# Optimization experiments

Measured on AMD Instinct MI355X. Metric: run time of the kernel, lower is better.

## Reference

```python
import jax, jax.numpy as jnp
import numpy as np

N_NODES = 100000
N_EDGES = 3200000
DIMS = [64, 64, 32, 16]  # [embedding_size] + conv_dim_list
LN_EPS = 1e-5


def _xavier(key, shape):
    fan_in, fan_out = shape[0], shape[1]
    s = np.sqrt(6.0 / (fan_in + fan_out)).astype(np.float32)
    return jax.random.uniform(key, shape, jnp.float32, -s, s)


def _layer_norm(x, g, b):
    m = jnp.mean(x, axis=-1, keepdims=True)
    v = jnp.mean((x - m) ** 2, axis=-1, keepdims=True)
    return (x - m) * jax.lax.rsqrt(v + LN_EPS) * g + b


def _bi_interaction(ego, rows, cols, vals, w1, b1, w2, b2, g1, be1, g2, be2):
    # sparse SpMM: side = A_in @ ego, A_in[rows, cols] = vals
    msg = vals[:, None] * ego[cols]                              # (E, d_in)
    side = jax.ops.segment_sum(msg, rows, num_segments=ego.shape[0])
    s = _layer_norm(jax.nn.leaky_relu((ego + side) @ w1 + b1), g1, be1)
    bi = _layer_norm(jax.nn.leaky_relu((ego * side) @ w2 + b2), g2, be2)
    return s + bi


def _l2_normalize(x):
    n = jnp.sqrt(jnp.sum(x * x, axis=1, keepdims=True))
    return x / jnp.maximum(n, 1e-12)


def setup_inputs() -> dict:
    key = jax.random.key(0)
    ks = jax.random.split(key, 32)
    inp = {
        "emb": jax.random.normal(ks[0], (N_NODES, DIMS[0]), jnp.float32) * 0.1,
        "rows": jax.random.randint(ks[1], (N_EDGES,), 0, N_NODES, jnp.int32),
        "cols": jax.random.randint(ks[2], (N_EDGES,), 0, N_NODES, jnp.int32),
        "vals": jax.random.uniform(ks[3], (N_EDGES,), jnp.float32),
    }
    i = 4
    for k in range(3):
        din, dout = DIMS[k], DIMS[k + 1]
        inp[f"w1_{k}"] = _xavier(ks[i], (din, dout)); i += 1
        inp[f"b1_{k}"] = jnp.zeros((dout,), jnp.float32)
        inp[f"w2_{k}"] = _xavier(ks[i], (din, dout)); i += 1
        inp[f"b2_{k}"] = jnp.zeros((dout,), jnp.float32)
        inp[f"g1_{k}"] = jnp.ones((dout,), jnp.float32)
        inp[f"be1_{k}"] = jnp.zeros((dout,), jnp.float32)
        inp[f"g2_{k}"] = jnp.ones((dout,), jnp.float32)
        inp[f"be2_{k}"] = jnp.zeros((dout,), jnp.float32)
    return inp


def reference(emb, rows, cols, vals,
              w1_0, b1_0, w2_0, b2_0, g1_0, be1_0, g2_0, be2_0,
              w1_1, b1_1, w2_1, b2_1, g1_1, be1_1, g2_1, be2_1,
              w1_2, b1_2, w2_2, b2_2, g1_2, be1_2, g2_2, be2_2):
    layers = [
        (w1_0, b1_0, w2_0, b2_0, g1_0, be1_0, g2_0, be2_0),
        (w1_1, b1_1, w2_1, b2_1, g1_1, be1_1, g2_1, be2_1),
        (w1_2, b1_2, w2_2, b2_2, g1_2, be1_2, g2_2, be2_2),
    ]
    ego = emb
    all_embed = [ego]
    for p in layers:
        ego = _bi_interaction(ego, rows, cols, vals, *p)
        all_embed.append(_l2_normalize(ego))
    return jnp.concatenate(all_embed, axis=1)  # (N, 64+64+32+16)
```

## Files before the change

kernel.cpp:

```cpp
#include <hip/hip_runtime.h>
#include <hip/hip_fp16.h>

#define N_NODES 100000
#define N_EDGES 3200000
#define OUT_DIM 176
#define LN_EPS 1e-5f

typedef _Float16 h2 __attribute__((ext_vector_type(2)));

#define NBUCK 196
#define PC_BLOCKS 512
#define PC_CHUNK (N_EDGES / PC_BLOCKS)
#define BP_CHUNK 4096
#define BP_BLOCKS ((N_EDGES + BP_CHUNK - 1) / BP_CHUNK)

__global__ __launch_bounds__(256) void convert_emb_kernel(
    const float* __restrict__ emb, float* __restrict__ out,
    __half* __restrict__ emb_h) {
  int t = blockIdx.x * blockDim.x + threadIdx.x;
  if (t < N_NODES * 16) {
    int n = t >> 4, q = t & 15;
    float4 v = ((const float4*)emb)[t];
    ((float4*)out)[n * 44 + q] = v;
    __half2 a = __floats2half2_rn(v.x, v.y);
    __half2 b = __floats2half2_rn(v.z, v.w);
    uint2 u;
    u.x = *(unsigned int*)&a;
    u.y = *(unsigned int*)&b;
    ((uint2*)emb_h)[t] = u;
  }
}

__global__ __launch_bounds__(256) void wprep_all_kernel(
    const float* __restrict__ w1_0, const float* __restrict__ w2_0,
    const float* __restrict__ w1_1, const float* __restrict__ w2_1,
    const float* __restrict__ w1_2, const float* __restrict__ w2_2,
    __half* __restrict__ wt1_0, __half* __restrict__ wt2_0,
    __half* __restrict__ wt1_1, __half* __restrict__ wt2_1,
    __half* __restrict__ wt1_2, __half* __restrict__ wt2_2) {
  int idx = blockIdx.x * 256 + threadIdx.x;
  const float* w1;
  const float* w2;
  __half* t1;
  __half* t2;
  int din, dout;
  if (idx < 4096) {
    w1 = w1_0; w2 = w2_0; t1 = wt1_0; t2 = wt2_0; din = 64; dout = 64;
  } else if (idx < 4096 + 2048) {
    idx -= 4096;
    w1 = w1_1; w2 = w2_1; t1 = wt1_1; t2 = wt2_1; din = 64; dout = 32;
  } else if (idx < 4096 + 2048 + 512) {
    idx -= 4096 + 2048;
    w1 = w1_2; w2 = w2_2; t1 = wt1_2; t2 = wt2_2; din = 32; dout = 16;
  } else {
    return;
  }
  int i = idx / dout, j = idx % dout;
  t1[j * din + i] = __float2half(w1[idx]);
  t2[j * din + i] = __float2half(w2[idx]);
}

__global__ __launch_bounds__(256) void precount_kernel(
    const int* __restrict__ rows, int* __restrict__ gcount) {
  __shared__ int hist[NBUCK];
  for (int i = threadIdx.x; i < NBUCK; i += 256) hist[i] = 0;
  __syncthreads();
  const int e0 = blockIdx.x * PC_CHUNK;
  for (int e = e0 + threadIdx.x; e < e0 + PC_CHUNK; e += 256) {
    const int r = __builtin_nontemporal_load(rows + e);
    atomicAdd(&hist[r >> 9], 1);
  }
  __syncthreads();
  for (int i = threadIdx.x; i < NBUCK; i += 256)
    if (hist[i]) atomicAdd(&gcount[i], hist[i]);
}

__global__ __launch_bounds__(256) void bucket_scan_kernel(
    const int* __restrict__ gcount, int* __restrict__ bucket_base,
    int* __restrict__ bucket_cursor) {
  __shared__ int sA[256], sB[256];
  const int t = threadIdx.x;
  int v = (t < NBUCK) ? gcount[t] : 0;
  sA[t] = v;
  __syncthreads();
  int* src = sA;
  int* dst = sB;
  for (int off = 1; off < 256; off <<= 1) {
    dst[t] = src[t] + ((t >= off) ? src[t - off] : 0);
    __syncthreads();
    int* tmp = src; src = dst; dst = tmp;
  }
  if (t < NBUCK) {
    const int excl = src[t] - v;
    bucket_base[t] = excl;
    bucket_cursor[t] = excl;
  }
  if (t == 0) bucket_base[NBUCK] = N_EDGES;
}

__global__ __launch_bounds__(256) void bucket_pass_kernel(
    const int* __restrict__ rows, const int* __restrict__ cols,
    const float* __restrict__ vals, int* __restrict__ bucket_cursor,
    int2* __restrict__ bucketed) {
  __shared__ int cnt[NBUCK], cur[NBUCK], gbase[NBUCK];
  for (int i = threadIdx.x; i < NBUCK; i += 256) {
    cnt[i] = 0;
    cur[i] = 0;
  }
  __syncthreads();

  const int e0 = blockIdx.x * BP_CHUNK;
  int r_[16], c_[16];
  float v_[16];
#pragma unroll
  for (int k = 0; k < 16; ++k) {
    const int e = e0 + threadIdx.x + k * 256;
    if (e < N_EDGES) {
      r_[k] = rows[e];
      c_[k] = cols[e];
      v_[k] = vals[e];
      atomicAdd(&cnt[r_[k] >> 9], 1);
    } else {
      r_[k] = -1;
    }
  }
  __syncthreads();

  for (int i = threadIdx.x; i < NBUCK; i += 256)
    gbase[i] = cnt[i] ? atomicAdd(&bucket_cursor[i], cnt[i]) : 0;
  __syncthreads();

#pragma unroll
  for (int k = 0; k < 16; ++k) {
    if (r_[k] >= 0) {
      const int b = r_[k] >> 9;
      const int lp = atomicAdd(&cur[b], 1);
      const int meta = c_[k] | ((r_[k] & 511) << 17);
      bucketed[gbase[b] + lp] = make_int2(meta, __float_as_int(v_[k]));
    }
  }
}

__global__ __launch_bounds__(512) void csr_build_kernel(
    const int2* __restrict__ bucketed, const int* __restrict__ bucket_base,
    int* __restrict__ row_ptr, int2* __restrict__ packed) {
  __shared__ int hist[512], cur[512], sA[512], sB[512];
  const int t = threadIdx.x;
  const int blk = blockIdx.x;
  const int base = bucket_base[blk];
  const int n = bucket_base[blk + 1] - base;

  hist[t] = 0;
  __syncthreads();
  for (int i = t; i < n; i += 512) {
    const int rlow = bucketed[base + i].x >> 17;
    atomicAdd(&hist[rlow], 1);
  }
  __syncthreads();

  sA[t] = hist[t];
  __syncthreads();
  int* src = sA;
  int* dst = sB;
  for (int off = 1; off < 512; off <<= 1) {
    dst[t] = src[t] + ((t >= off) ? src[t - off] : 0);
    __syncthreads();
    int* tmp = src; src = dst; dst = tmp;
  }
  const int excl = src[t] - hist[t];

  const int row0 = blk << 9;
  if (row0 + t < N_NODES) row_ptr[row0 + t] = base + excl;
  if (blk == NBUCK - 1 && t == 0) row_ptr[N_NODES] = N_EDGES;
  cur[t] = excl;
  __syncthreads();

  for (int i = t; i < n; i += 512) {
    const int2 m = bucketed[base + i];
    const int rlow = m.x >> 17;
    const int col = m.x & 0x1FFFF;
    const int p = atomicAdd(&cur[rlow], 1);
    packed[base + p] = make_int2(col, m.y);
  }
}

template <int DIN>
__global__ __launch_bounds__(512) void spmm_kernel(
    const __half* __restrict__ ego_h, const int* __restrict__ row_ptr,
    const long long* __restrict__ packed, __half* __restrict__ side_out_h) {
  constexpr int LPH = DIN / 8;
  constexpr int NGRP = 64 / LPH;

  const int lane = threadIdx.x & 63;
  const int li = lane % LPH;
  const int grp = lane / LPH;
  const int node = (blockIdx.x * blockDim.x + threadIdx.x) >> 6;
  if (node >= N_NODES) return;

  const uint4* __restrict__ ego8 = (const uint4*)ego_h;
  const int start = row_ptr[node];
  const int end = row_ptr[node + 1];

  float s[8] = {0.f, 0.f, 0.f, 0.f, 0.f, 0.f, 0.f, 0.f};

  for (int base = start; base < end; base += 64) {
    const int idx = base + lane;
    long long m = 0;
    if (idx < end) m = __builtin_nontemporal_load(packed + idx);
    int mc = (int)m;
    int mv = (int)(m >> 32);
    const int cnt = min(end - base, 64);
    const int kmax = (cnt + NGRP - 1) / NGRP;
    for (int k = 0; k < kmax; ++k) {
      const int src = k * NGRP + grp;
      const int c = __shfl(mc, src, 64);
      const float v = __int_as_float(__shfl(mv, src, 64));
      uint4 raw = ego8[(long)c * LPH + li];
      const __half2* hp = (const __half2*)&raw;
      const float2 f0 = __half22float2(hp[0]);
      const float2 f1 = __half22float2(hp[1]);
      const float2 f2 = __half22float2(hp[2]);
      const float2 f3 = __half22float2(hp[3]);
      s[0] += v * f0.x; s[1] += v * f0.y;
      s[2] += v * f1.x; s[3] += v * f1.y;
      s[4] += v * f2.x; s[5] += v * f2.y;
      s[6] += v * f3.x; s[7] += v * f3.y;
    }
  }

#pragma unroll
  for (int mask = LPH; mask < 64; mask <<= 1) {
#pragma unroll
    for (int r = 0; r < 8; ++r) s[r] += __shfl_xor(s[r], mask, 64);
  }

  if (grp == 0) {
    __half2 p0 = __floats2half2_rn(s[0], s[1]);
    __half2 p1 = __floats2half2_rn(s[2], s[3]);
    __half2 p2 = __floats2half2_rn(s[4], s[5]);
    __half2 p3 = __floats2half2_rn(s[6], s[7]);
    uint4 u;
    u.x = *(unsigned int*)&p0;
    u.y = *(unsigned int*)&p1;
    u.z = *(unsigned int*)&p2;
    u.w = *(unsigned int*)&p3;
    ((uint4*)side_out_h)[(long)node * LPH + li] = u;
  }
}

template <int DIN, int DOUT, int COL_OFF>
__global__ __launch_bounds__(256, 4) void dense_kernel(
    const __half* __restrict__ ego_h, const __half* __restrict__ side_h,
    const __half* __restrict__ w1t, const float* __restrict__ b1,
    const __half* __restrict__ w2t, const float* __restrict__ b2,
    const float* __restrict__ g1, const float* __restrict__ be1,
    const float* __restrict__ g2, const float* __restrict__ be2,
    __half* __restrict__ ego_h_out, float* __restrict__ out) {
  constexpr int CH = DIN / 8;
  constexpr int G = 64 / CH;
  constexpr int NPW = 64 / DOUT;
  constexpr int PASSES = G / NPW;

  const int lane = threadIdx.x & 63;
  const int w = threadIdx.x >> 6;
  const int j = lane % DOUT;
  const int sub = lane / DOUT;
  const int sn = lane / CH;
  const int sc = lane % CH;

  __shared__ uint4 lds[4][2][64];

  const uint4* __restrict__ w1u = (const uint4*)w1t;
  const uint4* __restrict__ w2u = (const uint4*)w2t;
  uint4 wraw1[CH], wraw2[CH];
#pragma unroll
  for (int q = 0; q < CH; ++q) {
    wraw1[q] = w1u[j * CH + q];
    wraw2[q] = w2u[j * CH + q];
  }
  const float bb1 = b1[j], bb2 = b2[j];
  const float gg1 = g1[j], gg2 = g2[j];
  const float bbe1 = be1[j], bbe2 = be2[j];

  const uint4* __restrict__ ego8 = (const uint4*)ego_h;
  const uint4* __restrict__ side8 = (const uint4*)side_h;

  const int waveId = (blockIdx.x * blockDim.x + threadIdx.x) >> 6;
  const int nwaves = (gridDim.x * blockDim.x) >> 6;
  const int ngangs = N_NODES / G;

  uint4 eR, sR;
  if (waveId < ngangs) {
    const size_t b = (size_t)(waveId * G + sn) * CH + sc;
    eR = ego8[b];
    sR = side8[b];
  }

  for (int gang = waveId; gang < ngangs; gang += nwaves) {
    uint4 xsU, xpU;
    {
      const h2* e2 = (const h2*)&eR;
      const h2* s2 = (const h2*)&sR;
      h2* xs2 = (h2*)&xsU;
      h2* xp2 = (h2*)&xpU;
#pragma unroll
      for (int r = 0; r < 4; ++r) {
        xs2[r] = e2[r] + s2[r];
        xp2[r] = e2[r] * s2[r];
      }
    }
    asm volatile("s_waitcnt lgkmcnt(0)" ::: "memory");
    __builtin_amdgcn_sched_barrier(0);
    lds[w][0][lane] = xsU;
    lds[w][1][lane] = xpU;

    const int gn = gang + nwaves;
    if (gn < ngangs) {
      const size_t b = (size_t)(gn * G + sn) * CH + sc;
      eR = ego8[b];
      sR = side8[b];
    }

    asm volatile("s_waitcnt lgkmcnt(0)" ::: "memory");
    __builtin_amdgcn_sched_barrier(0);

#pragma unroll
    for (int p = 0; p < PASSES; ++p) {
      const int nin = p * NPW + sub;
      const int node = gang * G + nin;

      float a1a = bb1, a1b = 0.f, a2a = bb2, a2b = 0.f;
#pragma unroll
      for (int q = 0; q < CH; ++q) {
        uint4 xsq = lds[w][0][nin * CH + q];
        uint4 xpq = lds[w][1][nin * CH + q];
        const h2* xs2 = (const h2*)&xsq;
        const h2* xp2 = (const h2*)&xpq;
        const h2* wq1 = (const h2*)&wraw1[q];
        const h2* wq2 = (const h2*)&wraw2[q];
#pragma unroll
        for (int r = 0; r < 4; ++r) {
#if __has_builtin(__builtin_amdgcn_fdot2)
          if (q & 1) {
            a1b = __builtin_amdgcn_fdot2(xs2[r], wq1[r], a1b, false);
            a2b = __builtin_amdgcn_fdot2(xp2[r], wq2[r], a2b, false);
          } else {
            a1a = __builtin_amdgcn_fdot2(xs2[r], wq1[r], a1a, false);
            a2a = __builtin_amdgcn_fdot2(xp2[r], wq2[r], a2a, false);
          }
#else
          if (q & 1) {
            a1b += (float)xs2[r].x * (float)wq1[r].x +
                   (float)xs2[r].y * (float)wq1[r].y;
            a2b += (float)xp2[r].x * (float)wq2[r].x +
                   (float)xp2[r].y * (float)wq2[r].y;
          } else {
            a1a += (float)xs2[r].x * (float)wq1[r].x +
                   (float)xs2[r].y * (float)wq1[r].y;
            a2a += (float)xp2[r].x * (float)wq2[r].x +
                   (float)xp2[r].y * (float)wq2[r].y;
          }
#endif
        }
      }

      const float acc1 = a1a + a1b;
      const float acc2 = a2a + a2b;
      const float h1 = acc1 > 0.f ? acc1 : 0.01f * acc1;
      const float h2v = acc2 > 0.f ? acc2 : 0.01f * acc2;

      float s1 = h1, q1 = h1 * h1, s2 = h2v, q2 = h2v * h2v;
#pragma unroll
      for (int mask = DOUT / 2; mask > 0; mask >>= 1) {
        s1 += __shfl_xor(s1, mask, DOUT);
        q1 += __shfl_xor(q1, mask, DOUT);
        s2 += __shfl_xor(s2, mask, DOUT);
        q2 += __shfl_xor(q2, mask, DOUT);
      }
      const float m1 = s1 * (1.0f / DOUT);
      const float m2 = s2 * (1.0f / DOUT);
      const float v1 = fmaxf(q1 * (1.0f / DOUT) - m1 * m1, 0.f);
      const float v2 = fmaxf(q2 * (1.0f / DOUT) - m2 * m2, 0.f);
      const float sv = (h1 - m1) * rsqrtf(v1 + LN_EPS) * gg1 + bbe1;
      const float bv = (h2v - m2) * rsqrtf(v2 + LN_EPS) * gg2 + bbe2;
      const float en = sv + bv;

      float ss = en * en;
#pragma unroll
      for (int mask = DOUT / 2; mask > 0; mask >>= 1) {
        ss += __shfl_xor(ss, mask, DOUT);
      }
      const float ov = en / fmaxf(sqrtf(ss), 1e-12f);

      if (ego_h_out) ego_h_out[(long)node * DOUT + j] = __float2half(en);
      out[(long)node * OUT_DIM + COL_OFF + j] = ov;
    }
  }
}

extern "C" void kernel_launch(void* const* d_in, const int* in_sizes, int n_in,
                              void* d_out, int out_size, void* d_ws,
                              size_t ws_size, hipStream_t stream) {
  const float* emb = (const float*)d_in[0];
  const int* rows = (const int*)d_in[1];
  const int* cols = (const int*)d_in[2];
  const float* vals = (const float*)d_in[3];

  const float* P[3][8];
  for (int k = 0; k < 3; ++k)
    for (int p = 0; p < 8; ++p) P[k][p] = (const float*)d_in[4 + 8 * k + p];

  float* out = (float*)d_out;

  char* ws = (char*)d_ws;
  int2* packed = (int2*)ws;
  char* sideArea = ws + (size_t)N_EDGES * 8;
  __half* side_h = (__half*)sideArea;
  int2* bucketed = (int2*)sideArea;
  __half* emb_h = (__half*)(sideArea + (size_t)N_NODES * 64 * 4);
  __half* ego1_h = emb_h + (size_t)N_NODES * 64;
  __half* ego2_h = ego1_h + (size_t)N_NODES * 64;
  __half* wt1_0 = ego2_h + (size_t)N_NODES * 32;
  __half* wt2_0 = wt1_0 + 4096;
  __half* wt1_1 = wt2_0 + 4096;
  __half* wt2_1 = wt1_1 + 2048;
  __half* wt1_2 = wt2_1 + 2048;
  __half* wt2_2 = wt1_2 + 512;
  int* row_ptr = (int*)(wt2_2 + 512);
  int* gcount = row_ptr + (N_NODES + 1);
  int* bucket_base = gcount + NBUCK;
  int* bucket_cursor = bucket_base + (NBUCK + 1);

  hipMemsetAsync(gcount, 0, NBUCK * sizeof(int), stream);
  precount_kernel<<<PC_BLOCKS, 256, 0, stream>>>(rows, gcount);
  bucket_scan_kernel<<<1, 256, 0, stream>>>(gcount, bucket_base,
                                            bucket_cursor);
  bucket_pass_kernel<<<BP_BLOCKS, 256, 0, stream>>>(rows, cols, vals,
                                                    bucket_cursor, bucketed);
  csr_build_kernel<<<NBUCK, 512, 0, stream>>>(bucketed, bucket_base, row_ptr,
                                              packed);

  wprep_all_kernel<<<26, 256, 0, stream>>>(P[0][0], P[0][2], P[1][0], P[1][2],
                                           P[2][0], P[2][2], wt1_0, wt2_0,
                                           wt1_1, wt2_1, wt1_2, wt2_2);

  convert_emb_kernel<<<(N_NODES * 16 + 255) / 256, 256, 0, stream>>>(emb, out,
                                                                     emb_h);

  const int SPMM_BLOCKS = (N_NODES + 7) / 8;
  const int DENSE_BLOCKS = 2048;

  spmm_kernel<64><<<SPMM_BLOCKS, 512, 0, stream>>>(
      emb_h, row_ptr, (const long long*)packed, side_h);
  dense_kernel<64, 64, 64><<<DENSE_BLOCKS, 256, 0, stream>>>(
      emb_h, side_h, wt1_0, P[0][1], wt2_0, P[0][3], P[0][4], P[0][5],
      P[0][6], P[0][7], ego1_h, out);

  spmm_kernel<64><<<SPMM_BLOCKS, 512, 0, stream>>>(
      ego1_h, row_ptr, (const long long*)packed, side_h);
  dense_kernel<64, 32, 128><<<DENSE_BLOCKS, 256, 0, stream>>>(
      ego1_h, side_h, wt1_1, P[1][1], wt2_1, P[1][3], P[1][4], P[1][5],
      P[1][6], P[1][7], ego2_h, out);

  spmm_kernel<32><<<SPMM_BLOCKS, 512, 0, stream>>>(
      ego2_h, row_ptr, (const long long*)packed, side_h);
  dense_kernel<32, 16, 160><<<DENSE_BLOCKS, 256, 0, stream>>>(
      ego2_h, side_h, wt1_2, P[2][1], wt2_2, P[2][3], P[2][4], P[2][5],
      P[2][6], P[2][7], nullptr, out);
}
```

Baseline: 536.1 us.

## Fuse SpMM and dense bi-interaction into one per-layer kernel

Merges the sparse aggregation and the dense linear/LayerNorm/L2 step into a single persistent kernel per layer. Each wave gathers neighbours for one node, combines the result with the node's embedding in registers, stages it through LDS, and runs the matvec with the weights split across lane groups, finishing with a cross-group shuffle reduction. This removes the fp16 side buffer round trip and three kernel launches. In exchange, the dense phase now processes one node per wave, so only a fraction of lanes do useful work there, and the fixed grid sizes may limit how well latency is hidden during the gather.

```diff
diff --git a/kernel.cpp b/kernel.cpp
--- a/kernel.cpp
+++ b/kernel.cpp
@@ -184,214 +184,164 @@
   }
 }
 
-template <int DIN>
-__global__ __launch_bounds__(512) void spmm_kernel(
+template <int DIN, int DOUT, int COL_OFF>
+__global__ __launch_bounds__(256, 4) void fused_layer_kernel(
     const __half* __restrict__ ego_h, const int* __restrict__ row_ptr,
-    const long long* __restrict__ packed, __half* __restrict__ side_out_h) {
+    const long long* __restrict__ packed, const __half* __restrict__ w1t,
+    const float* __restrict__ b1, const __half* __restrict__ w2t,
+    const float* __restrict__ b2, const float* __restrict__ g1,
+    const float* __restrict__ be1, const float* __restrict__ g2,
+    const float* __restrict__ be2, __half* __restrict__ ego_h_out,
+    float* __restrict__ out) {
   constexpr int LPH = DIN / 8;
   constexpr int NGRP = 64 / LPH;
+  constexpr int CH = DIN / 8;
+  constexpr int SPL = 64 / DOUT;
+  constexpr int QPS = CH / SPL;
 
   const int lane = threadIdx.x & 63;
+  const int w = threadIdx.x >> 6;
   const int li = lane % LPH;
   const int grp = lane / LPH;
-  const int node = (blockIdx.x * blockDim.x + threadIdx.x) >> 6;
-  if (node >= N_NODES) return;
-
-  const uint4* __restrict__ ego8 = (const uint4*)ego_h;
-  const int start = row_ptr[node];
-  const int end = row_ptr[node + 1];
-
-  float s[8] = {0.f, 0.f, 0.f, 0.f, 0.f, 0.f, 0.f, 0.f};
-
-  for (int base = start; base < end; base += 64) {
-    const int idx = base + lane;
-    long long m = 0;
-    if (idx < end) m = __builtin_nontemporal_load(packed + idx);
-    int mc = (int)m;
-    int mv = (int)(m >> 32);
-    const int cnt = min(end - base, 64);
-    const int kmax = (cnt + NGRP - 1) / NGRP;
-    for (int k = 0; k < kmax; ++k) {
-      const int src = k * NGRP + grp;
-      const int c = __shfl(mc, src, 64);
-      const float v = __int_as_float(__shfl(mv, src, 64));
-      uint4 raw = ego8[(long)c * LPH + li];
-      const __half2* hp = (const __half2*)&raw;
-      const float2 f0 = __half22float2(hp[0]);
-      const float2 f1 = __half22float2(hp[1]);
-      const float2 f2 = __half22float2(hp[2]);
-      const float2 f3 = __half22float2(hp[3]);
-      s[0] += v * f0.x; s[1] += v * f0.y;
-      s[2] += v * f1.x; s[3] += v * f1.y;
-      s[4] += v * f2.x; s[5] += v * f2.y;
-      s[6] += v * f3.x; s[7] += v * f3.y;
-    }
-  }
-
-#pragma unroll
-  for (int mask = LPH; mask < 64; mask <<= 1) {
-#pragma unroll
-    for (int r = 0; r < 8; ++r) s[r] += __shfl_xor(s[r], mask, 64);
-  }
-
-  if (grp == 0) {
-    __half2 p0 = __floats2half2_rn(s[0], s[1]);
-    __half2 p1 = __floats2half2_rn(s[2], s[3]);
-    __half2 p2 = __floats2half2_rn(s[4], s[5]);
-    __half2 p3 = __floats2half2_rn(s[6], s[7]);
-    uint4 u;
-    u.x = *(unsigned int*)&p0;
-    u.y = *(unsigned int*)&p1;
-    u.z = *(unsigned int*)&p2;
-    u.w = *(unsigned int*)&p3;
-    ((uint4*)side_out_h)[(long)node * LPH + li] = u;
-  }
-}
-
-template <int DIN, int DOUT, int COL_OFF>
-__global__ __launch_bounds__(256, 4) void dense_kernel(
-    const __half* __restrict__ ego_h, const __half* __restrict__ side_h,
-    const __half* __restrict__ w1t, const float* __restrict__ b1,
-    const __half* __restrict__ w2t, const float* __restrict__ b2,
-    const float* __restrict__ g1, const float* __restrict__ be1,
-    const float* __restrict__ g2, const float* __restrict__ be2,
-    __half* __restrict__ ego_h_out, float* __restrict__ out) {
-  constexpr int CH = DIN / 8;
-  constexpr int G = 64 / CH;
-  constexpr int NPW = 64 / DOUT;
-  constexpr int PASSES = G / NPW;
-
-  const int lane = threadIdx.x & 63;
-  const int w = threadIdx.x >> 6;
   const int j = lane % DOUT;
   const int sub = lane / DOUT;
-  const int sn = lane / CH;
-  const int sc = lane % CH;
-
-  __shared__ uint4 lds[4][2][64];
+
+  __shared__ uint4 lds[4][2][CH];
 
   const uint4* __restrict__ w1u = (const uint4*)w1t;
   const uint4* __restrict__ w2u = (const uint4*)w2t;
-  uint4 wraw1[CH], wraw2[CH];
-#pragma unroll
-  for (int q = 0; q < CH; ++q) {
-    wraw1[q] = w1u[j * CH + q];
-    wraw2[q] = w2u[j * CH + q];
+  uint4 wr1[QPS], wr2[QPS];
+#pragma unroll
+  for (int q = 0; q < QPS; ++q) {
+    wr1[q] = w1u[j * CH + sub * QPS + q];
+    wr2[q] = w2u[j * CH + sub * QPS + q];
+    asm volatile("" : "+v"(wr1[q].x), "+v"(wr1[q].y), "+v"(wr1[q].z),
+                      "+v"(wr1[q].w));
+    asm volatile("" : "+v"(wr2[q].x), "+v"(wr2[q].y), "+v"(wr2[q].z),
+                      "+v"(wr2[q].w));
   }
   const float bb1 = b1[j], bb2 = b2[j];
   const float gg1 = g1[j], gg2 = g2[j];
   const float bbe1 = be1[j], bbe2 = be2[j];
 
   const uint4* __restrict__ ego8 = (const uint4*)ego_h;
-  const uint4* __restrict__ side8 = (const uint4*)side_h;
 
   const int waveId = (blockIdx.x * blockDim.x + threadIdx.x) >> 6;
   const int nwaves = (gridDim.x * blockDim.x) >> 6;
-  const int ngangs = N_NODES / G;
-
-  uint4 eR, sR;
-  if (waveId < ngangs) {
-    const size_t b = (size_t)(waveId * G + sn) * CH + sc;
-    eR = ego8[b];
-    sR = side8[b];
-  }
-
-  for (int gang = waveId; gang < ngangs; gang += nwaves) {
-    uint4 xsU, xpU;
-    {
-      const h2* e2 = (const h2*)&eR;
-      const h2* s2 = (const h2*)&sR;
-      h2* xs2 = (h2*)&xsU;
-      h2* xp2 = (h2*)&xpU;
-#pragma unroll
-      for (int r = 0; r < 4; ++r) {
-        xs2[r] = e2[r] + s2[r];
-        xp2[r] = e2[r] * s2[r];
+
+  for (int node = waveId; node < N_NODES; node += nwaves) {
+    const int start = row_ptr[node];
+    const int end = row_ptr[node + 1];
+
+    float s[8] = {0.f, 0.f, 0.f, 0.f, 0.f, 0.f, 0.f, 0.f};
+    for (int base = start; base < end; base += 64) {
+      const int idx = base + lane;
+      long long m = 0;
+      if (idx < end) m = __builtin_nontemporal_load(packed + idx);
+      const int mc = (int)m;
+      const int mv = (int)(m >> 32);
+      const int cnt = min(end - base, 64);
+      const int kmax = (cnt + NGRP - 1) / NGRP;
+      for (int k = 0; k < kmax; ++k) {
+        const int src = k * NGRP + grp;
+        const int c = __shfl(mc, src, 64);
+        const float v = __int_as_float(__shfl(mv, src, 64));
+        uint4 raw = ego8[(long)c * LPH + li];
+        const __half2* hp = (const __half2*)&raw;
+        const float2 f0 = __half22float2(hp[0]);
+        const float2 f1 = __half22float2(hp[1]);
+        const float2 f2 = __half22float2(hp[2]);
+        const float2 f3 = __half22float2(hp[3]);
+        s[0] += v * f0.x; s[1] += v * f0.y;
+        s[2] += v * f1.x; s[3] += v * f1.y;
+        s[4] += v * f2.x; s[5] += v * f2.y;
+        s[6] += v * f3.x; s[7] += v * f3.y;
       }
     }
+
+    uint4 eg = make_uint4(0, 0, 0, 0);
+    if (grp == 0) eg = ego8[(long)node * CH + li];
+
+#pragma unroll
+    for (int mask = LPH; mask < 64; mask <<= 1)
+#pragma unroll
+      for (int r = 0; r < 8; ++r) s[r] += __shfl_xor(s[r], mask, 64);
+
     asm volatile("s_waitcnt lgkmcnt(0)" ::: "memory");
     __builtin_amdgcn_sched_barrier(0);
-    lds[w][0][lane] = xsU;
-    lds[w][1][lane] = xpU;
-
-    const int gn = gang + nwaves;
-    if (gn < ngangs) {
-      const size_t b = (size_t)(gn * G + sn) * CH + sc;
-      eR = ego8[b];
-      sR = side8[b];
-    }
-
+    if (grp == 0) {
+      const __half2* ep = (const __half2*)&eg;
+      uint4 xsU, xpU;
+      __half2* xs2 = (__half2*)&xsU;
+      __half2* xp2 = (__half2*)&xpU;
+#pragma unroll
+      for (int r = 0; r < 4; ++r) {
+        const float2 ef = __half22float2(ep[r]);
+        xs2[r] = __floats2half2_rn(ef.x + s[2 * r], ef.y + s[2 * r + 1]);
+        xp2[r] = __floats2half2_rn(ef.x * s[2 * r], ef.y * s[2 * r + 1]);
+      }
+      lds[w][0][li] = xsU;
+      lds[w][1][li] = xpU;
+    }
     asm volatile("s_waitcnt lgkmcnt(0)" ::: "memory");
     __builtin_amdgcn_sched_barrier(0);
 
-#pragma unroll
-    for (int p = 0; p < PASSES; ++p) {
-      const int nin = p * NPW + sub;
-      const int node = gang * G + nin;
-
-      float a1a = bb1, a1b = 0.f, a2a = bb2, a2b = 0.f;
-#pragma unroll
-      for (int q = 0; q < CH; ++q) {
-        uint4 xsq = lds[w][0][nin * CH + q];
-        uint4 xpq = lds[w][1][nin * CH + q];
-        const h2* xs2 = (const h2*)&xsq;
-        const h2* xp2 = (const h2*)&xpq;
-        const h2* wq1 = (const h2*)&wraw1[q];
-        const h2* wq2 = (const h2*)&wraw2[q];
-#pragma unroll
-        for (int r = 0; r < 4; ++r) {
+    float a1 = (sub == 0) ? bb1 : 0.f;
+    float a2 = (sub == 0) ? bb2 : 0.f;
+#pragma unroll
+    for (int q = 0; q < QPS; ++q) {
+      uint4 xsq = lds[w][0][sub * QPS + q];
+      uint4 xpq = lds[w][1][sub * QPS + q];
+      const h2* xs2 = (const h2*)&xsq;
+      const h2* xp2 = (const h2*)&xpq;
+      const h2* wq1 = (const h2*)&wr1[q];
+      const h2* wq2 = (const h2*)&wr2[q];
+#pragma unroll
+      for (int r = 0; r < 4; ++r) {
 #if __has_builtin(__builtin_amdgcn_fdot2)
-          if (q & 1) {
-            a1b = __builtin_amdgcn_fdot2(xs2[r], wq1[r], a1b, false);
-            a2b = __builtin_amdgcn_fdot2(xp2[r], wq2[r], a2b, false);
-          } else {
-            a1a = __builtin_amdgcn_fdot2(xs2[r], wq1[r], a1a, false);
-            a2a = __builtin_amdgcn_fdot2(xp2[r], wq2[r], a2a, false);
-          }
+        a1 = __builtin_amdgcn_fdot2(xs2[r], wq1[r], a1, false);
+        a2 = __builtin_amdgcn_fdot2(xp2[r], wq2[r], a2, false);
 #else
-          if (q & 1) {
-            a1b += (float)xs2[r].x * (float)wq1[r].x +
-                   (float)xs2[r].y * (float)wq1[r].y;
-            a2b += (float)xp2[r].x * (float)wq2[r].x +
-                   (float)xp2[r].y * (float)wq2[r].y;
-          } else {
-            a1a += (float)xs2[r].x * (float)wq1[r].x +
-                   (float)xs2[r].y * (float)wq1[r].y;
-            a2a += (float)xp2[r].x * (float)wq2[r].x +
-                   (float)xp2[r].y * (float)wq2[r].y;
-          }
+        a1 += (float)xs2[r].x * (float)wq1[r].x +
+              (float)xs2[r].y * (float)wq1[r].y;
+        a2 += (float)xp2[r].x * (float)wq2[r].x +
+              (float)xp2[r].y * (float)wq2[r].y;
 #endif
-        }
       }
-
-      const float acc1 = a1a + a1b;
-      const float acc2 = a2a + a2b;
-      const float h1 = acc1 > 0.f ? acc1 : 0.01f * acc1;
-      const float h2v = acc2 > 0.f ? acc2 : 0.01f * acc2;
-
-      float s1 = h1, q1 = h1 * h1, s2 = h2v, q2 = h2v * h2v;
-#pragma unroll
-      for (int mask = DOUT / 2; mask > 0; mask >>= 1) {
-        s1 += __shfl_xor(s1, mask, DOUT);
-        q1 += __shfl_xor(q1, mask, DOUT);
-        s2 += __shfl_xor(s2, mask, DOUT);
-        q2 += __shfl_xor(q2, mask, DOUT);
-      }
-      const float m1 = s1 * (1.0f / DOUT);
-      const float m2 = s2 * (1.0f / DOUT);
-      const float v1 = fmaxf(q1 * (1.0f / DOUT) - m1 * m1, 0.f);
-      const float v2 = fmaxf(q2 * (1.0f / DOUT) - m2 * m2, 0.f);
-      const float sv = (h1 - m1) * rsqrtf(v1 + LN_EPS) * gg1 + bbe1;
-      const float bv = (h2v - m2) * rsqrtf(v2 + LN_EPS) * gg2 + bbe2;
-      const float en = sv + bv;
-
-      float ss = en * en;
-#pragma unroll
-      for (int mask = DOUT / 2; mask > 0; mask >>= 1) {
-        ss += __shfl_xor(ss, mask, DOUT);
-      }
-      const float ov = en / fmaxf(sqrtf(ss), 1e-12f);
-
+    }
+#pragma unroll
+    for (int mk = DOUT; mk < 64; mk <<= 1) {
+      a1 += __shfl_xor(a1, mk, 64);
+      a2 += __shfl_xor(a2, mk, 64);
+    }
+
+    const float h1 = a1 > 0.f ? a1 : 0.01f * a1;
+    const float h2v = a2 > 0.f ? a2 : 0.01f * a2;
+
+    float s1 = h1, q1 = h1 * h1, s2 = h2v, q2 = h2v * h2v;
+#pragma unroll
+    for (int mask = DOUT / 2; mask > 0; mask >>= 1) {
+      s1 += __shfl_xor(s1, mask, DOUT);
+      q1 += __shfl_xor(q1, mask, DOUT);
+      s2 += __shfl_xor(s2, mask, DOUT);
+      q2 += __shfl_xor(q2, mask, DOUT);
+    }
+    const float m1 = s1 * (1.0f / DOUT);
+    const float m2 = s2 * (1.0f / DOUT);
+    const float v1 = fmaxf(q1 * (1.0f / DOUT) - m1 * m1, 0.f);
+    const float v2 = fmaxf(q2 * (1.0f / DOUT) - m2 * m2, 0.f);
+    const float sv = (h1 - m1) * rsqrtf(v1 + LN_EPS) * gg1 + bbe1;
+    const float bv = (h2v - m2) * rsqrtf(v2 + LN_EPS) * gg2 + bbe2;
+    const float en = sv + bv;
+
+    float ss = en * en;
+#pragma unroll
+    for (int mask = DOUT / 2; mask > 0; mask >>= 1) {
+      ss += __shfl_xor(ss, mask, DOUT);
+    }
+    const float ov = en / fmaxf(sqrtf(ss), 1e-12f);
+
+    if (sub == 0) {
       if (ego_h_out) ego_h_out[(long)node * DOUT + j] = __float2half(en);
       out[(long)node * OUT_DIM + COL_OFF + j] = ov;
     }
@@ -415,7 +365,6 @@
   char* ws = (char*)d_ws;
   int2* packed = (int2*)ws;
   char* sideArea = ws + (size_t)N_EDGES * 8;
-  __half* side_h = (__half*)sideArea;
   int2* bucketed = (int2*)sideArea;
   __half* emb_h = (__half*)(sideArea + (size_t)N_NODES * 64 * 4);
   __half* ego1_h = emb_h + (size_t)N_NODES * 64;
@@ -447,24 +396,15 @@
   convert_emb_kernel<<<(N_NODES * 16 + 255) / 256, 256, 0, stream>>>(emb, out,
                                                                      emb_h);
 
-  const int SPMM_BLOCKS = (N_NODES + 7) / 8;
-  const int DENSE_BLOCKS = 2048;
-
-  spmm_kernel<64><<<SPMM_BLOCKS, 512, 0, stream>>>(
-      emb_h, row_ptr, (const long long*)packed, side_h);
-  dense_kernel<64, 64, 64><<<DENSE_BLOCKS, 256, 0, stream>>>(
-      emb_h, side_h, wt1_0, P[0][1], wt2_0, P[0][3], P[0][4], P[0][5],
-      P[0][6], P[0][7], ego1_h, out);
-
-  spmm_kernel<64><<<SPMM_BLOCKS, 512, 0, stream>>>(
-      ego1_h, row_ptr, (const long long*)packed, side_h);
-  dense_kernel<64, 32, 128><<<DENSE_BLOCKS, 256, 0, stream>>>(
-      ego1_h, side_h, wt1_1, P[1][1], wt2_1, P[1][3], P[1][4], P[1][5],
-      P[1][6], P[1][7], ego2_h, out);
-
-  spmm_kernel<32><<<SPMM_BLOCKS, 512, 0, stream>>>(
-      ego2_h, row_ptr, (const long long*)packed, side_h);
-  dense_kernel<32, 16, 160><<<DENSE_BLOCKS, 256, 0, stream>>>(
-      ego2_h, side_h, wt1_2, P[2][1], wt2_2, P[2][3], P[2][4], P[2][5],
-      P[2][6], P[2][7], nullptr, out);
-}
+  fused_layer_kernel<64, 64, 64><<<1024, 256, 0, stream>>>(
+      emb_h, row_ptr, (const long long*)packed, wt1_0, P[0][1], wt2_0,
+      P[0][3], P[0][4], P[0][5], P[0][6], P[0][7], ego1_h, out);
+
+  fused_layer_kernel<64, 32, 128><<<2048, 256, 0, stream>>>(
+      ego1_h, row_ptr, (const long long*)packed, wt1_1, P[1][1], wt2_1,
+      P[1][3], P[1][4], P[1][5], P[1][6], P[1][7], ego2_h, out);
+
+  fused_layer_kernel<32, 16, 160><<<2048, 256, 0, stream>>>(
+      ego2_h, row_ptr, (const long long*)packed, wt1_2, P[2][1], wt2_2,
+      P[2][3], P[2][4], P[2][5], P[2][6], P[2][7], nullptr, out);
+}
```

New measurement: 619.3 us. +15.5%, slower.
